# Kernel tuning notes

Measured on AMD Instinct MI355X. Metric: run time of the kernel, lower is better.

## Reference

```python
import jax, jax.numpy as jnp
import numpy as np

B, S, E, H = 2, 2048, 1024, 16
DK = E // H


def setup_inputs() -> dict:
    key = jax.random.key(0)
    ks = jax.random.split(key, 8)
    scale = 1.0 / np.sqrt(E)
    inp = {
        "query": jax.random.normal(ks[0], (B, S, E), jnp.float32),
        "key": jax.random.normal(ks[1], (B, S, E), jnp.float32),
        "value": jax.random.normal(ks[2], (B, S, E), jnp.float32),
        # causal mask: True = masked out (upper triangle)
        "attn_mask": jnp.triu(jnp.ones((S, S), jnp.bool_), k=1),
        "Wq": jax.random.normal(ks[3], (E, E), jnp.float32) * scale,
        "bq": jnp.zeros((E,), jnp.float32),
        "Wk": jax.random.normal(ks[4], (E, E), jnp.float32) * scale,
        "bk": jnp.zeros((E,), jnp.float32),
        "Wv": jax.random.normal(ks[5], (E, E), jnp.float32) * scale,
        "bv": jnp.zeros((E,), jnp.float32),
        "Wo": jax.random.normal(ks[6], (E, E), jnp.float32) * scale,
        "bo": jnp.zeros((E,), jnp.float32),
    }
    return inp


def reference(query, key, value, attn_mask, Wq, bq, Wk, bk, Wv, bv, Wo, bo):
    bs = query.shape[0]
    # QKV projections, split heads: [B,S,E] -> [B,H,S,DK]
    def proj(x, W, b):
        y = jnp.einsum('bse,ef->bsf', x, W) + b
        return y.reshape(bs, -1, H, DK).transpose(0, 2, 1, 3)

    q = proj(query, Wq, bq)
    k = proj(key, Wk, bk)
    v = proj(value, Wv, bv)

    # scaled dot-product attention with additive -1e9 mask fill
    scores = jnp.einsum('bhqd,bhkd->bhqk', q, k) / np.sqrt(DK).astype(jnp.float32)
    scores = jnp.where(attn_mask[None, None, :, :], jnp.float32(-1e9), scores)
    attn = jax.nn.softmax(scores, axis=-1)
    ctx = jnp.einsum('bhqk,bhkd->bhqd', attn, v)  # [B,H,S,DK]

    concat = ctx.transpose(0, 2, 1, 3).reshape(bs, -1, E)  # [B,S,E]
    return jnp.einsum('bse,ef->bsf', concat, Wo) + bo
```

## Files before the change

### kernel.cpp

```cpp
#include <hip/hip_runtime.h>
#include <hip/hip_bf16.h>

typedef __attribute__((ext_vector_type(8))) short bf16x8;
typedef __attribute__((ext_vector_type(4))) float f32x4;

constexpr int Bc = 2, Sc = 2048, Ec = 1024, Hc = 16, DKc = 64;

__device__ __forceinline__ unsigned short f2b(float f) {
    union { float f; unsigned u; } v; v.f = f;
    unsigned u = v.u;
    return (unsigned short)((u + 0x7FFFu + ((u >> 16) & 1u)) >> 16);
}
__device__ __forceinline__ unsigned short f2bn(float f) {
    return __bfloat16_as_ushort(__float2bfloat16(f));
}
__device__ __forceinline__ float b2f(unsigned short h) {
    union { unsigned u; float f; } v; v.u = ((unsigned)h) << 16;
    return v.f;
}

#define GLOAD16(ldsp, gp)                                                                  \
    __builtin_amdgcn_global_load_lds((const __attribute__((address_space(1))) void*)(gp),  \
                                     (__attribute__((address_space(3))) void*)(ldsp),      \
                                     16, 0, 0)

#define ASM_VM8 asm volatile("s_waitcnt vmcnt(8)" ::: "memory")
#define ASM_VM4 asm volatile("s_waitcnt vmcnt(4)" ::: "memory")
#define ASM_VM0 asm volatile("s_waitcnt vmcnt(0)" ::: "memory")
#define ASM_LG0 asm volatile("s_waitcnt lgkmcnt(0)" ::: "memory")
#define ASM_BAR asm volatile("s_barrier" ::: "memory")

__global__ __launch_bounds__(256) void conv_x(
    const float* __restrict__ Xq, const float* __restrict__ Xk, const float* __restrict__ Xv,
    unsigned short* __restrict__ Xb)
{
    const int z = blockIdx.y;
    const float* X = (z == 0) ? Xq : (z == 1) ? Xk : Xv;
    unsigned short* O = Xb + (size_t)z * 4194304;
    const int n4 = 4194304 / 4;
    for (int i = blockIdx.x * 256 + threadIdx.x; i < n4; i += gridDim.x * 256) {
        float4 v = ((const float4*)X)[i];
        ushort4 h; h.x = f2b(v.x); h.y = f2b(v.y); h.z = f2b(v.z); h.w = f2b(v.w);
        ((ushort4*)O)[i] = h;
    }
}

__global__ __launch_bounds__(256) void conv_w(
    const float* __restrict__ Wq, const float* __restrict__ Wk,
    const float* __restrict__ Wv, const float* __restrict__ Wo,
    unsigned short* __restrict__ Wt)
{
    const int z = blockIdx.z;
    const float* W = (z == 0) ? Wq : (z == 1) ? Wk : (z == 2) ? Wv : Wo;
    unsigned short* O = Wt + (size_t)z * 1048576;
    __shared__ unsigned short T[64][65];
    const int k0 = blockIdx.y * 64, n0 = blockIdx.x * 64;
    const int tx = threadIdx.x & 15, ty = threadIdx.x >> 4;
    #pragma unroll
    for (int p = 0; p < 4; p++) {
        float4 v = *(const float4*)&W[(size_t)(k0 + ty + 16 * p) * 1024 + n0 + 4 * tx];
        T[ty + 16 * p][4 * tx + 0] = f2b(v.x);
        T[ty + 16 * p][4 * tx + 1] = f2b(v.y);
        T[ty + 16 * p][4 * tx + 2] = f2b(v.z);
        T[ty + 16 * p][4 * tx + 3] = f2b(v.w);
    }
    __syncthreads();
    #pragma unroll
    for (int p = 0; p < 4; p++) {
        ushort4 o;
        o.x = T[4 * tx + 0][ty + 16 * p];
        o.y = T[4 * tx + 1][ty + 16 * p];
        o.z = T[4 * tx + 2][ty + 16 * p];
        o.w = T[4 * tx + 3][ty + 16 * p];
        *(ushort4*)&O[(size_t)(n0 + ty + 16 * p) * 1024 + k0 + 4 * tx] = o;
    }
}

#define GEMM_STAGE(buf, kk)                                                                \
    _Pragma("unroll")                                                                      \
    for (int i = 0; i < 2; i++) {                                                          \
        const int rb = 32 * w + 16 * i;                                                    \
        GLOAD16(SMEM[buf] + rb * 32, Ag + (size_t)(m0 + rb + lr) * 1024 + (kk) + lcs);     \
        GLOAD16(SMEM[3 + (buf)] + rb * 32, Bg + (size_t)(n0 + rb + lr) * 1024 + (kk) + lcs); \
    }

#define GEMM_CORE_CV                                                                       \
    GEMM_STAGE(0, 0)                                                                       \
    GEMM_STAGE(1, 32)                                                                      \
    GEMM_STAGE(2, 64)                                                                      \
    for (int t = 0; t < 32; t++) {                                                         \
        const int cur = t % 3;                                                             \
        if (t < 30) { ASM_VM8; } else if (t == 30) { ASM_VM4; } else { ASM_VM0; }          \
        ASM_BAR;                                                                           \
        bf16x8 a[4], b[4];                                                                 \
        _Pragma("unroll")                                                                  \
        for (int m = 0; m < 4; m++)                                                        \
            a[m] = *(const bf16x8*)((const char*)SMEM[cur] +                               \
                   (wr + 16 * m + c) * 64 + ((g ^ ((c >> 1) & 3)) << 4));                  \
        _Pragma("unroll")                                                                  \
        for (int n = 0; n < 4; n++)                                                        \
            b[n] = *(const bf16x8*)((const char*)SMEM[3 + cur] +                           \
                   (wc + 16 * n + c) * 64 + ((g ^ ((c >> 1) & 3)) << 4));                  \
        ASM_LG0;                                                                           \
        ASM_BAR;                                                                           \
        if (t + 3 < 32) { GEMM_STAGE(cur, (t + 3) * 32) }                                  \
        __builtin_amdgcn_s_setprio(1);                                                     \
        _Pragma("unroll")                                                                  \
        for (int m = 0; m < 4; m++)                                                        \
            _Pragma("unroll")                                                              \
            for (int n = 0; n < 4; n++)                                                    \
                acc[m][n] = __builtin_amdgcn_mfma_f32_16x16x32_bf16(a[m], b[n], acc[m][n], 0, 0, 0); \
        __builtin_amdgcn_s_setprio(0);                                                     \
    }

__global__ __launch_bounds__(256) void gemm_qkv(
    const unsigned short* __restrict__ Xb, const unsigned short* __restrict__ Wt,
    const float* __restrict__ bq, const float* __restrict__ bk, const float* __restrict__ bv,
    unsigned short* __restrict__ Qw, unsigned short* __restrict__ Kw,
    unsigned short* __restrict__ Vt)
{
    const int wgid = blockIdx.x;
    const int xcd = wgid & 7, slot = wgid >> 3;
    const int y = xcd + 8 * (slot & 3);
    const int xz = slot >> 2;
    const int x = xz & 7, z = xz >> 3;

    const unsigned short* Ag = Xb + (size_t)z * 4194304;
    const unsigned short* Bg = Wt + (size_t)z * 1048576;
    const float* bias = (z == 0) ? bq : (z == 1) ? bk : bv;

    __shared__ __align__(16) unsigned short SMEM[6][4096];

    const int tid = threadIdx.x;
    const int m0 = y * 128, n0 = x * 128;
    const int lane = tid & 63, c = lane & 15, g = lane >> 4;
    const int w = tid >> 6;
    const int wr = (w >> 1) * 64, wc = (w & 1) * 64;
    const int lr = lane >> 2;
    const int lcs = ((lane & 3) ^ ((lane >> 3) & 3)) * 8;

    f32x4 acc[4][4] = {};
    GEMM_CORE_CV

    if (z == 2) {
        unsigned short* Tr = &SMEM[0][0];
        ASM_BAR;
        #pragma unroll
        for (int n = 0; n < 4; n++) {
            const int dl = wc + n * 16 + c;
            const float bv_ = bias[n0 + dl];
            #pragma unroll
            for (int m = 0; m < 4; m++) {
                const int sl = wr + m * 16 + 4 * g;
                ushort4 pw;
                pw.x = f2b(acc[m][n][0] + bv_);
                pw.y = f2b(acc[m][n][1] + bv_);
                pw.z = f2b(acc[m][n][2] + bv_);
                pw.w = f2b(acc[m][n][3] + bv_);
                const int sc = (sl >> 2) ^ (dl & 7);
                *(ushort4*)&Tr[dl * 128 + sc * 4] = pw;
            }
        }
        ASM_BAR;
        #pragma unroll
        for (int it = 0; it < 16; it++) {
            const int idx = it * 256 + tid;
            const int dl = idx >> 5;
            const int sc0 = idx & 31;
            const int sc = sc0 ^ (dl & 7);
            const ushort4 pw = *(const ushort4*)&Tr[dl * 128 + sc * 4];
            const int gn = n0 + dl;
            const int h = gn >> 6, d = gn & 63;
            const int gm = m0 + sc0 * 4;
            const int bb = gm >> 11, s = gm & 2047;
            *(ushort4*)&Vt[((size_t)(bb * Hc + h) * DKc + d) * Sc + s] = pw;
        }
    } else {
        #pragma unroll
        for (int n = 0; n < 4; n++) {
            const int gn = n0 + wc + n * 16 + c;
            const float bv_ = bias[gn];
            const int h = gn >> 6, d = gn & 63;
            #pragma unroll
            for (int m = 0; m < 4; m++) {
                #pragma unroll
                for (int r = 0; r < 4; r++) {
                    const int gm = m0 + wr + m * 16 + 4 * g + r;
                    const int bb = gm >> 11, s = gm & 2047;
                    const float val = acc[m][n][r] + bv_;
                    if (z == 0)
                        Qw[((size_t)(bb * Hc + h) * Sc + s) * DKc + d] = f2b(val * 0.125f);
                    else
                        Kw[((size_t)(bb * Hc + h) * Sc + s) * DKc + d] = f2b(val);
                }
            }
        }
    }
}

__global__ __launch_bounds__(256) void gemm_out(
    const unsigned short* __restrict__ Ctx, const unsigned short* __restrict__ Wt,
    const float* __restrict__ bo, float* __restrict__ Out)
{
    const int wgid = blockIdx.x;
    const int xcd = wgid & 7, slot = wgid >> 3;
    const int y = xcd + 8 * (slot & 3);
    const int x = slot >> 2;

    const unsigned short* Ag = Ctx;
    const unsigned short* Bg = Wt + (size_t)3 * 1048576;

    __shared__ __align__(16) unsigned short SMEM[6][4096];

    const int tid = threadIdx.x;
    const int m0 = y * 128, n0 = x * 128;
    const int lane = tid & 63, c = lane & 15, g = lane >> 4;
    const int w = tid >> 6;
    const int wr = (w >> 1) * 64, wc = (w & 1) * 64;
    const int lr = lane >> 2;
    const int lcs = ((lane & 3) ^ ((lane >> 3) & 3)) * 8;

    f32x4 acc[4][4] = {};
    GEMM_CORE_CV

    #pragma unroll
    for (int n = 0; n < 4; n++) {
        const int gn = n0 + wc + n * 16 + c;
        const float bv_ = bo[gn];
        #pragma unroll
        for (int m = 0; m < 4; m++) {
            #pragma unroll
            for (int r = 0; r < 4; r++) {
                const int gm = m0 + wr + m * 16 + 4 * g + r;
                Out[(size_t)gm * Ec + gn] = acc[m][n][r] + bv_;
            }
        }
    }
}

__global__ __launch_bounds__(256) void attn(
    const unsigned short* __restrict__ Qw, const unsigned short* __restrict__ Kw,
    const unsigned short* __restrict__ Vt,
    unsigned short* __restrict__ Opart, float* __restrict__ Lpart)
{
    const int bid = blockIdx.x;
    const int bh = bid & 31;
    const int ps = bid >> 5;
    const int pair = ps >> 1, sp = ps & 1;
    const int tid = threadIdx.x, w = tid >> 6, lane = tid & 63;
    const int c = lane & 15, g = lane >> 4;

    const unsigned short* Qh = Qw + (size_t)bh * Sc * DKc;
    const unsigned short* Kh = Kw + (size_t)bh * Sc * DKc;
    const unsigned short* Vh = Vt + (size_t)bh * DKc * Sc;

    __shared__ __align__(16) unsigned short Kl[4096];
    __shared__ __align__(16) unsigned short Vl[4096];
    __shared__ __align__(16) unsigned short Pl[4][16][72];

    const int lrow8 = lane >> 3;
    const int cbp = ((lane & 7) ^ lrow8) << 4;
    const int swz = (c & 7) << 4;

#define STAGE_KV(KV0)                                                                       \
    _Pragma("unroll")                                                                       \
    for (int s2 = 0; s2 < 2; s2++) {                                                        \
        const int row_ = s2 * 32 + w * 8 + lrow8;                                           \
        GLOAD16((char*)Kl + s2 * 4096 + w * 1024,                                           \
                (const char*)Kh + (size_t)((KV0) + row_) * 128 + cbp);                      \
        GLOAD16((char*)Vl + s2 * 4096 + w * 1024,                                           \
                (const char*)Vh + (size_t)row_ * 4096 + (size_t)(KV0) * 2 + cbp);           \
    }

    for (int half = 0; half < 2; half++) {
        const int qt = half ? (31 - pair) : pair;
        const int qbase = qt * 64;
        const int qrow = qbase + w * 16 + c;
        const int qtg = bh * 32 + qt;

        const bf16x8 q0 = *(const bf16x8*)&Qh[(size_t)qrow * DKc + 8 * g];
        const bf16x8 q1 = *(const bf16x8*)&Qh[(size_t)qrow * DKc + 32 + 8 * g];

        float lsum = 0.f;
        f32x4 o[4] = {};

        for (int j = sp; j <= qt; j += 2) {
            const int kv0 = j * 64;
            const bool maskt = (j == qt);

            STAGE_KV(kv0)
            __syncthreads();

            f32x4 d[4] = {};
            __builtin_amdgcn_s_setprio(1);
            #pragma unroll
            for (int t = 0; t < 4; t++) {
                const char* kb = (const char*)Kl + (16 * t + c) * 128;
                const bf16x8 k0 = *(const bf16x8*)(kb + ((16 * g) ^ swz));
                const bf16x8 k1 = *(const bf16x8*)(kb + ((64 + 16 * g) ^ swz));
                d[t] = __builtin_amdgcn_mfma_f32_16x16x32_bf16(k0, q0, d[t], 0, 0, 0);
                d[t] = __builtin_amdgcn_mfma_f32_16x16x32_bf16(k1, q1, d[t], 0, 0, 0);
            }
            __builtin_amdgcn_s_setprio(0);

            float s[16];
            if (maskt) {
                #pragma unroll
                for (int t = 0; t < 4; t++)
                    #pragma unroll
                    for (int r = 0; r < 4; r++) {
                        const int kv = kv0 + 16 * t + 4 * g + r;
                        s[4 * t + r] = __expf((kv <= qrow) ? d[t][r] : -1e30f);
                    }
            } else {
                #pragma unroll
                for (int t = 0; t < 4; t++)
                    #pragma unroll
                    for (int r = 0; r < 4; r++)
                        s[4 * t + r] = __expf(d[t][r]);
            }
            #pragma unroll
            for (int i = 0; i < 16; i++) lsum += s[i];

            #pragma unroll
            for (int t = 0; t < 4; t++) {
                ushort4 pw;
                pw.x = f2bn(s[4 * t + 0]); pw.y = f2bn(s[4 * t + 1]);
                pw.z = f2bn(s[4 * t + 2]); pw.w = f2bn(s[4 * t + 3]);
                *(ushort4*)&Pl[w][c][16 * t + 4 * g] = pw;
            }
            const bf16x8 pA0 = *(const bf16x8*)&Pl[w][c][8 * g];
            const bf16x8 pA1 = *(const bf16x8*)&Pl[w][c][32 + 8 * g];

            __builtin_amdgcn_s_setprio(1);
            #pragma unroll
            for (int ch = 0; ch < 4; ch++) {
                const char* vb = (const char*)Vl + (16 * ch + c) * 128;
                const bf16x8 v0 = *(const bf16x8*)(vb + ((16 * g) ^ swz));
                const bf16x8 v1 = *(const bf16x8*)(vb + ((64 + 16 * g) ^ swz));
                f32x4 t = o[ch];
                t = __builtin_amdgcn_mfma_f32_16x16x32_bf16(pA0, v0, t, 0, 0, 0);
                o[ch] = __builtin_amdgcn_mfma_f32_16x16x32_bf16(pA1, v1, t, 0, 0, 0);
            }
            __builtin_amdgcn_s_setprio(0);
            __syncthreads();
        }

        lsum += __shfl_xor(lsum, 16);
        lsum += __shfl_xor(lsum, 32);
        if (g == 0)
            Lpart[((size_t)sp * 1024 + qtg) * 64 + w * 16 + c] = lsum;

        #pragma unroll
        for (int ch = 0; ch < 4; ch++) {
            #pragma unroll
            for (int r = 0; r < 4; r++) {
                const int lrow = w * 16 + 4 * g + r;
                Opart[(((size_t)sp * 1024 + qtg) * 64 + lrow) * 64 + ch * 16 + c] =
                    f2bn(o[ch][r]);
            }
        }
    }
#undef STAGE_KV
}

__global__ __launch_bounds__(256) void attn_combine(
    const unsigned short* __restrict__ Opart, const float* __restrict__ Lpart,
    unsigned short* __restrict__ Ctx)
{
    const int qtg = blockIdx.x;
    const int bh = qtg >> 5, qt = qtg & 31;
    const int bb = bh >> 4, hh = bh & 15;
    #pragma unroll
    for (int it = 0; it < 2; it++) {
        const int chunk = threadIdx.x + it * 256;
        const int row = chunk >> 3, c8 = (chunk & 7) * 8;
        const size_t o0 = ((size_t)qtg * 64 + row) * 64 + c8;
        const size_t o1 = ((size_t)(1024 + qtg) * 64 + row) * 64 + c8;
        const bf16x8 a = *(const bf16x8*)&Opart[o0];
        const bf16x8 b = *(const bf16x8*)&Opart[o1];
        const float linv = 1.f / (Lpart[(size_t)qtg * 64 + row] +
                                  Lpart[(size_t)(1024 + qtg) * 64 + row]);
        ushort4 lo, hi;
        lo.x = f2bn((b2f((unsigned short)a[0]) + b2f((unsigned short)b[0])) * linv);
        lo.y = f2bn((b2f((unsigned short)a[1]) + b2f((unsigned short)b[1])) * linv);
        lo.z = f2bn((b2f((unsigned short)a[2]) + b2f((unsigned short)b[2])) * linv);
        lo.w = f2bn((b2f((unsigned short)a[3]) + b2f((unsigned short)b[3])) * linv);
        hi.x = f2bn((b2f((unsigned short)a[4]) + b2f((unsigned short)b[4])) * linv);
        hi.y = f2bn((b2f((unsigned short)a[5]) + b2f((unsigned short)b[5])) * linv);
        hi.z = f2bn((b2f((unsigned short)a[6]) + b2f((unsigned short)b[6])) * linv);
        hi.w = f2bn((b2f((unsigned short)a[7]) + b2f((unsigned short)b[7])) * linv);
        const int qg = qt * 64 + row;
        unsigned short* dst = &Ctx[((size_t)(bb * Sc + qg)) * Ec + hh * 64 + c8];
        *(ushort4*)dst = lo;
        *(ushort4*)(dst + 4) = hi;
    }
}

extern "C" void kernel_launch(void* const* d_in, const int* in_sizes, int n_in,
                              void* d_out, int out_size, void* d_ws, size_t ws_size,
                              hipStream_t stream) {
    const float* query = (const float*)d_in[0];
    const float* key   = (const float*)d_in[1];
    const float* value = (const float*)d_in[2];
    const float* Wq = (const float*)d_in[4];
    const float* bq = (const float*)d_in[5];
    const float* Wk = (const float*)d_in[6];
    const float* bk = (const float*)d_in[7];
    const float* Wv = (const float*)d_in[8];
    const float* bv = (const float*)d_in[9];
    const float* Wo = (const float*)d_in[10];
    const float* bo = (const float*)d_in[11];

    const size_t n_elem = (size_t)Bc * Hc * Sc * DKc;
    unsigned short* Qw = (unsigned short*)d_ws;
    unsigned short* Kw = Qw + n_elem;
    unsigned short* Vt = Kw + n_elem;
    unsigned short* Cx = Vt + n_elem;
    unsigned short* Xb = Cx + n_elem;
    unsigned short* Wt = Xb + 3 * n_elem;

    unsigned short* Opart = Xb;
    float* Lpart = (float*)(Xb + (size_t)2 * 1024 * 64 * 64);

    conv_x<<<dim3(512, 3), 256, 0, stream>>>(query, key, value, Xb);
    conv_w<<<dim3(16, 16, 4), 256, 0, stream>>>(Wq, Wk, Wv, Wo, Wt);
    gemm_qkv<<<dim3(768), 256, 0, stream>>>(Xb, Wt, bq, bk, bv, Qw, Kw, Vt);
    attn<<<dim3(1024), 256, 0, stream>>>(Qw, Kw, Vt, Opart, Lpart);
    attn_combine<<<dim3(1024), 256, 0, stream>>>(Opart, Lpart, Cx);
    gemm_out<<<dim3(256), 256, 0, stream>>>(Cx, Wt, bo, (float*)d_out);
}
```

Baseline: 109.8 us.

## Fuse fp32-to-bf16 activation conversion into QKV GEMM, double-buffer GEMM pipelines

Drops the separate conv_x kernel. gemm_qkv now loads fp32 activations straight into LDS (swizzled layout) and converts them to bf16 in registers before the MFMA, which removes a full read-write pass over the 3x8M-element input tensors. Both GEMMs move from triple to double buffering to fit the larger fp32 A tile, with adjusted vmcnt waits and a launch bound of 2 blocks per CU on gemm_qkv. The trade is twice the A-tile global and LDS traffic per k-step inside the GEMM, extra conversion ALU work, and a shallower prefetch depth.

```diff
diff --git a/kernel.cpp b/kernel.cpp
--- a/kernel.cpp
+++ b/kernel.cpp
@@ -24,26 +24,11 @@
                                      (__attribute__((address_space(3))) void*)(ldsp),      \
                                      16, 0, 0)
 
-#define ASM_VM8 asm volatile("s_waitcnt vmcnt(8)" ::: "memory")
+#define ASM_VM6 asm volatile("s_waitcnt vmcnt(6)" ::: "memory")
 #define ASM_VM4 asm volatile("s_waitcnt vmcnt(4)" ::: "memory")
 #define ASM_VM0 asm volatile("s_waitcnt vmcnt(0)" ::: "memory")
 #define ASM_LG0 asm volatile("s_waitcnt lgkmcnt(0)" ::: "memory")
 #define ASM_BAR asm volatile("s_barrier" ::: "memory")
-
-__global__ __launch_bounds__(256) void conv_x(
-    const float* __restrict__ Xq, const float* __restrict__ Xk, const float* __restrict__ Xv,
-    unsigned short* __restrict__ Xb)
-{
-    const int z = blockIdx.y;
-    const float* X = (z == 0) ? Xq : (z == 1) ? Xk : Xv;
-    unsigned short* O = Xb + (size_t)z * 4194304;
-    const int n4 = 4194304 / 4;
-    for (int i = blockIdx.x * 256 + threadIdx.x; i < n4; i += gridDim.x * 256) {
-        float4 v = ((const float4*)X)[i];
-        ushort4 h; h.x = f2b(v.x); h.y = f2b(v.y); h.z = f2b(v.z); h.w = f2b(v.w);
-        ((ushort4*)O)[i] = h;
-    }
-}
 
 __global__ __launch_bounds__(256) void conv_w(
     const float* __restrict__ Wq, const float* __restrict__ Wk,
@@ -76,45 +61,9 @@
     }
 }
 
-#define GEMM_STAGE(buf, kk)                                                                \
-    _Pragma("unroll")                                                                      \
-    for (int i = 0; i < 2; i++) {                                                          \
-        const int rb = 32 * w + 16 * i;                                                    \
-        GLOAD16(SMEM[buf] + rb * 32, Ag + (size_t)(m0 + rb + lr) * 1024 + (kk) + lcs);     \
-        GLOAD16(SMEM[3 + (buf)] + rb * 32, Bg + (size_t)(n0 + rb + lr) * 1024 + (kk) + lcs); \
-    }
-
-#define GEMM_CORE_CV                                                                       \
-    GEMM_STAGE(0, 0)                                                                       \
-    GEMM_STAGE(1, 32)                                                                      \
-    GEMM_STAGE(2, 64)                                                                      \
-    for (int t = 0; t < 32; t++) {                                                         \
-        const int cur = t % 3;                                                             \
-        if (t < 30) { ASM_VM8; } else if (t == 30) { ASM_VM4; } else { ASM_VM0; }          \
-        ASM_BAR;                                                                           \
-        bf16x8 a[4], b[4];                                                                 \
-        _Pragma("unroll")                                                                  \
-        for (int m = 0; m < 4; m++)                                                        \
-            a[m] = *(const bf16x8*)((const char*)SMEM[cur] +                               \
-                   (wr + 16 * m + c) * 64 + ((g ^ ((c >> 1) & 3)) << 4));                  \
-        _Pragma("unroll")                                                                  \
-        for (int n = 0; n < 4; n++)                                                        \
-            b[n] = *(const bf16x8*)((const char*)SMEM[3 + cur] +                           \
-                   (wc + 16 * n + c) * 64 + ((g ^ ((c >> 1) & 3)) << 4));                  \
-        ASM_LG0;                                                                           \
-        ASM_BAR;                                                                           \
-        if (t + 3 < 32) { GEMM_STAGE(cur, (t + 3) * 32) }                                  \
-        __builtin_amdgcn_s_setprio(1);                                                     \
-        _Pragma("unroll")                                                                  \
-        for (int m = 0; m < 4; m++)                                                        \
-            _Pragma("unroll")                                                              \
-            for (int n = 0; n < 4; n++)                                                    \
-                acc[m][n] = __builtin_amdgcn_mfma_f32_16x16x32_bf16(a[m], b[n], acc[m][n], 0, 0, 0); \
-        __builtin_amdgcn_s_setprio(0);                                                     \
-    }
-
-__global__ __launch_bounds__(256) void gemm_qkv(
-    const unsigned short* __restrict__ Xb, const unsigned short* __restrict__ Wt,
+__global__ __launch_bounds__(256, 2) void gemm_qkv(
+    const float* __restrict__ Xq, const float* __restrict__ Xk, const float* __restrict__ Xv,
+    const unsigned short* __restrict__ Wt,
     const float* __restrict__ bq, const float* __restrict__ bk, const float* __restrict__ bv,
     unsigned short* __restrict__ Qw, unsigned short* __restrict__ Kw,
     unsigned short* __restrict__ Vt)
@@ -125,25 +74,80 @@
     const int xz = slot >> 2;
     const int x = xz & 7, z = xz >> 3;
 
-    const unsigned short* Ag = Xb + (size_t)z * 4194304;
+    const float* Ag = (z == 0) ? Xq : (z == 1) ? Xk : Xv;
     const unsigned short* Bg = Wt + (size_t)z * 1048576;
     const float* bias = (z == 0) ? bq : (z == 1) ? bk : bv;
 
-    __shared__ __align__(16) unsigned short SMEM[6][4096];
+    __shared__ __align__(16) float SA[2][4096];
+    __shared__ __align__(16) unsigned short SB[2][4096];
 
     const int tid = threadIdx.x;
     const int m0 = y * 128, n0 = x * 128;
     const int lane = tid & 63, c = lane & 15, g = lane >> 4;
     const int w = tid >> 6;
     const int wr = (w >> 1) * 64, wc = (w & 1) * 64;
+    const int cc = c & 7;
+    const int arow = lane >> 3;
+    const int achk = ((lane & 7) ^ arow) << 4;
     const int lr = lane >> 2;
     const int lcs = ((lane & 3) ^ ((lane >> 3) & 3)) * 8;
 
+#define QKV_STAGE(buf, kk)                                                                 \
+    _Pragma("unroll")                                                                      \
+    for (int i = 0; i < 4; i++)                                                            \
+        GLOAD16((char*)SA[buf] + i * 4096 + w * 1024,                                      \
+                (const char*)Ag + (size_t)(m0 + 32 * i + 8 * w + arow) * 4096 +            \
+                (size_t)(kk) * 4 + achk);                                                  \
+    _Pragma("unroll")                                                                      \
+    for (int i = 0; i < 2; i++) {                                                          \
+        const int rb = 32 * w + 16 * i;                                                    \
+        GLOAD16(SB[buf] + rb * 32, Bg + (size_t)(n0 + rb + lr) * 1024 + (kk) + lcs);       \
+    }
+
     f32x4 acc[4][4] = {};
-    GEMM_CORE_CV
+    QKV_STAGE(0, 0)
+    QKV_STAGE(1, 32)
+    for (int t = 0; t < 32; t++) {
+        const int cur = t & 1;
+        if (t < 31) { ASM_VM6; } else { ASM_VM0; }
+        ASM_BAR;
+        f32x4 afr[4][2];
+        bf16x8 b[4];
+        #pragma unroll
+        for (int m = 0; m < 4; m++) {
+            const char* ab = (const char*)SA[cur] + (wr + 16 * m + c) * 128;
+            afr[m][0] = *(const f32x4*)(ab + (((2 * g) ^ cc) << 4));
+            afr[m][1] = *(const f32x4*)(ab + (((2 * g + 1) ^ cc) << 4));
+        }
+        #pragma unroll
+        for (int n = 0; n < 4; n++)
+            b[n] = *(const bf16x8*)((const char*)SB[cur] +
+                   (wc + 16 * n + c) * 64 + ((g ^ ((c >> 1) & 3)) << 4));
+        ASM_LG0;
+        ASM_BAR;
+        if (t + 2 < 32) { QKV_STAGE(cur, (t + 2) * 32) }
+        bf16x8 a[4];
+        #pragma unroll
+        for (int m = 0; m < 4; m++) {
+            bf16x8 av;
+            av[0] = (short)f2bn(afr[m][0][0]); av[1] = (short)f2bn(afr[m][0][1]);
+            av[2] = (short)f2bn(afr[m][0][2]); av[3] = (short)f2bn(afr[m][0][3]);
+            av[4] = (short)f2bn(afr[m][1][0]); av[5] = (short)f2bn(afr[m][1][1]);
+            av[6] = (short)f2bn(afr[m][1][2]); av[7] = (short)f2bn(afr[m][1][3]);
+            a[m] = av;
+        }
+        __builtin_amdgcn_s_setprio(1);
+        #pragma unroll
+        for (int m = 0; m < 4; m++)
+            #pragma unroll
+            for (int n = 0; n < 4; n++)
+                acc[m][n] = __builtin_amdgcn_mfma_f32_16x16x32_bf16(a[m], b[n], acc[m][n], 0, 0, 0);
+        __builtin_amdgcn_s_setprio(0);
+    }
+#undef QKV_STAGE
 
     if (z == 2) {
-        unsigned short* Tr = &SMEM[0][0];
+        unsigned short* Tr = (unsigned short*)&SA[0][0];
         ASM_BAR;
         #pragma unroll
         for (int n = 0; n < 4; n++) {
@@ -153,10 +157,10 @@
             for (int m = 0; m < 4; m++) {
                 const int sl = wr + m * 16 + 4 * g;
                 ushort4 pw;
-                pw.x = f2b(acc[m][n][0] + bv_);
-                pw.y = f2b(acc[m][n][1] + bv_);
-                pw.z = f2b(acc[m][n][2] + bv_);
-                pw.w = f2b(acc[m][n][3] + bv_);
+                pw.x = f2bn(acc[m][n][0] + bv_);
+                pw.y = f2bn(acc[m][n][1] + bv_);
+                pw.z = f2bn(acc[m][n][2] + bv_);
+                pw.w = f2bn(acc[m][n][3] + bv_);
                 const int sc = (sl >> 2) ^ (dl & 7);
                 *(ushort4*)&Tr[dl * 128 + sc * 4] = pw;
             }
@@ -189,9 +193,9 @@
                     const int bb = gm >> 11, s = gm & 2047;
                     const float val = acc[m][n][r] + bv_;
                     if (z == 0)
-                        Qw[((size_t)(bb * Hc + h) * Sc + s) * DKc + d] = f2b(val * 0.125f);
+                        Qw[((size_t)(bb * Hc + h) * Sc + s) * DKc + d] = f2bn(val * 0.125f);
                     else
-                        Kw[((size_t)(bb * Hc + h) * Sc + s) * DKc + d] = f2b(val);
+                        Kw[((size_t)(bb * Hc + h) * Sc + s) * DKc + d] = f2bn(val);
                 }
             }
         }
@@ -210,7 +214,7 @@
     const unsigned short* Ag = Ctx;
     const unsigned short* Bg = Wt + (size_t)3 * 1048576;
 
-    __shared__ __align__(16) unsigned short SMEM[6][4096];
+    __shared__ __align__(16) unsigned short SMEM[4][4096];
 
     const int tid = threadIdx.x;
     const int m0 = y * 128, n0 = x * 128;
@@ -220,8 +224,42 @@
     const int lr = lane >> 2;
     const int lcs = ((lane & 3) ^ ((lane >> 3) & 3)) * 8;
 
+#define OUT_STAGE(buf, kk)                                                                 \
+    _Pragma("unroll")                                                                      \
+    for (int i = 0; i < 2; i++) {                                                          \
+        const int rb = 32 * w + 16 * i;                                                    \
+        GLOAD16(SMEM[buf] + rb * 32, Ag + (size_t)(m0 + rb + lr) * 1024 + (kk) + lcs);     \
+        GLOAD16(SMEM[2 + (buf)] + rb * 32, Bg + (size_t)(n0 + rb + lr) * 1024 + (kk) + lcs); \
+    }
+
     f32x4 acc[4][4] = {};
-    GEMM_CORE_CV
+    OUT_STAGE(0, 0)
+    OUT_STAGE(1, 32)
+    for (int t = 0; t < 32; t++) {
+        const int cur = t & 1;
+        if (t < 31) { ASM_VM4; } else { ASM_VM0; }
+        ASM_BAR;
+        bf16x8 a[4], b[4];
+        #pragma unroll
+        for (int m = 0; m < 4; m++)
+            a[m] = *(const bf16x8*)((const char*)SMEM[cur] +
+                   (wr + 16 * m + c) * 64 + ((g ^ ((c >> 1) & 3)) << 4));
+        #pragma unroll
+        for (int n = 0; n < 4; n++)
+            b[n] = *(const bf16x8*)((const char*)SMEM[2 + cur] +
+                   (wc + 16 * n + c) * 64 + ((g ^ ((c >> 1) & 3)) << 4));
+        ASM_LG0;
+        ASM_BAR;
+        if (t + 2 < 32) { OUT_STAGE(cur, (t + 2) * 32) }
+        __builtin_amdgcn_s_setprio(1);
+        #pragma unroll
+        for (int m = 0; m < 4; m++)
+            #pragma unroll
+            for (int n = 0; n < 4; n++)
+                acc[m][n] = __builtin_amdgcn_mfma_f32_16x16x32_bf16(a[m], b[n], acc[m][n], 0, 0, 0);
+        __builtin_amdgcn_s_setprio(0);
+    }
+#undef OUT_STAGE
 
     #pragma unroll
     for (int n = 0; n < 4; n++) {
@@ -417,15 +455,14 @@
     unsigned short* Kw = Qw + n_elem;
     unsigned short* Vt = Kw + n_elem;
     unsigned short* Cx = Vt + n_elem;
-    unsigned short* Xb = Cx + n_elem;
-    unsigned short* Wt = Xb + 3 * n_elem;
-
-    unsigned short* Opart = Xb;
-    float* Lpart = (float*)(Xb + (size_t)2 * 1024 * 64 * 64);
-
-    conv_x<<<dim3(512, 3), 256, 0, stream>>>(query, key, value, Xb);
+    unsigned short* Sp = Cx + n_elem;
+    unsigned short* Wt = Sp + 3 * n_elem;
+
+    unsigned short* Opart = Sp;
+    float* Lpart = (float*)(Sp + (size_t)2 * 1024 * 64 * 64);
+
     conv_w<<<dim3(16, 16, 4), 256, 0, stream>>>(Wq, Wk, Wv, Wo, Wt);
-    gemm_qkv<<<dim3(768), 256, 0, stream>>>(Xb, Wt, bq, bk, bv, Qw, Kw, Vt);
+    gemm_qkv<<<dim3(768), 256, 0, stream>>>(query, key, value, Wt, bq, bk, bv, Qw, Kw, Vt);
     attn<<<dim3(1024), 256, 0, stream>>>(Qw, Kw, Vt, Opart, Lpart);
     attn_combine<<<dim3(1024), 256, 0, stream>>>(Opart, Lpart, Cx);
     gemm_out<<<dim3(256), 256, 0, stream>>>(Cx, Wt, bo, (float*)d_out);
```

Result: faster. 101.1 us, median of 3 (-7.9%).
